# Optimization experiments

Hardware: AMD Instinct MI355X
Metric: run time of the kernel (lower is better)

## Reference

```python
import jax, jax.numpy as jnp
import numpy as np

B, C, H, W = 4, 512, 64, 64
CQ = C // 8  # query/key channels


def setup_inputs() -> dict:
    key = jax.random.key(0)
    k1, k2, k3, k4 = jax.random.split(key, 4)
    x = jax.random.normal(k1, (B, C, H, W), dtype=jnp.float32)
    Wq = jax.random.normal(k2, (CQ, C), dtype=jnp.float32) * (1.0 / np.sqrt(C))
    Wk = jax.random.normal(k3, (CQ, C), dtype=jnp.float32) * (1.0 / np.sqrt(C))
    Wv = jax.random.normal(k4, (C, C), dtype=jnp.float32) * (1.0 / np.sqrt(C))
    gamma = jnp.ones((1,), dtype=jnp.float32)
    return {"x": x, "Wq": Wq, "Wk": Wk, "Wv": Wv, "gamma": gamma}


def reference(x, Wq, Wk, Wv, gamma):
    b, c, h, w = x.shape
    n = h * w
    xf = x.reshape(b, c, n)                      # [B, C, N]
    # 1x1 convs over the flattened spatial dim == per-position linear maps
    f = jnp.einsum('oc,bcn->bon', Wq, xf)        # [B, C/8, N] query
    g = jnp.einsum('oc,bcn->bon', Wk, xf)        # [B, C/8, N] key
    hv = jnp.einsum('oc,bcn->bon', Wv, xf)       # [B, C,   N] value
    # scores[b, i, j] = sum_k f[b,k,i] * g[b,k,j]  (f^T g)
    scores = jnp.einsum('bki,bkj->bij', f, g)    # [B, N, N]
    # torch softmax dim=1 -> normalize over the i axis (first N axis)
    beta = jax.nn.softmax(scores, axis=1)
    o = gamma[0] * jnp.einsum('bcn,bnj->bcj', hv, beta) + xf  # [B, C, N]
    return o.reshape(b, c, h, w)
```

## Files before the change

kernel.cpp:

```cpp
#include <hip/hip_runtime.h>
#include <hip/hip_bf16.h>

typedef unsigned short u16;
typedef unsigned int   u32;
typedef _Float16 f16;
typedef __attribute__((ext_vector_type(8))) _Float16 f16x8;
typedef __attribute__((ext_vector_type(4))) _Float16 f16x4;
typedef __attribute__((ext_vector_type(4))) float    f32x4;
typedef __attribute__((ext_vector_type(8))) unsigned short u16x8;

#define BATCH 4
#define CH 512
#define NN 4096
#define CQ 64
#define LOG2E 1.44269504f

__device__ __forceinline__ float bf2f(u16 v) {
    union { unsigned int u; float f; } x; x.u = ((unsigned int)v) << 16; return x.f;
}

__device__ __forceinline__ size_t stt_idx(int j, int i) {
    return (size_t)(j >> 4) * 65536 + (size_t)((i >> 3) * 128 + (j & 15) * 8 + (i & 7));
}

__device__ __forceinline__ void glds16(const f16* g, f16* s) {
    __builtin_amdgcn_global_load_lds(
        (const __attribute__((address_space(1))) void*)g,
        (__attribute__((address_space(3))) void*)s, 16, 0, 0);
}

__global__ __launch_bounds__(64) void detect_kernel(const u32* __restrict__ xw,
                                                    int* __restrict__ flag)
{
    const u32 w  = xw[threadIdx.x];
    const u32 ex = (w >> 23) & 0xFFu;
    const int plausible = (ex >= 100u && ex <= 132u) ? 1 : 0;
    const unsigned long long m = __ballot(plausible);
    if (threadIdx.x == 0) flag[0] = (__popcll(m) >= 48) ? 0 : 1;
}

__global__ __launch_bounds__(256) void wconv_kernel(
    const void* __restrict__ Wq, const void* __restrict__ Wk,
    const void* __restrict__ Wv, const int* __restrict__ flag,
    f16* __restrict__ Wc)
{
    const int isbf = *flag;
    const int row = blockIdx.x;
    const int t   = threadIdx.x;
    const void* src; int r;
    if (row < 64)       { src = Wq; r = row; }
    else if (row < 128) { src = Wk; r = row - 64; }
    else                { src = Wv; r = row - 128; }
    f16 v0, v1;
    if (isbf) {
        const u16* p = (const u16*)src + (size_t)r * CH + 2 * t;
        v0 = (f16)bf2f(p[0]); v1 = (f16)bf2f(p[1]);
    } else {
        const float* p = (const float*)src + (size_t)r * CH + 2 * t;
        v0 = (f16)p[0]; v1 = (f16)p[1];
    }
    Wc[(size_t)row * CH + 2 * t]     = v0;
    Wc[(size_t)row * CH + 2 * t + 1] = v1;
}

__global__ __launch_bounds__(256) void xpose_kernel(
    const void* __restrict__ xin, const int* __restrict__ flag,
    f16* __restrict__ xT)
{
    const int isbf = *flag;
    const int n0 = blockIdx.x * 64, c0 = blockIdx.y * 64, b = blockIdx.z;
    const int t  = threadIdx.x;
    __shared__ float Xl[64][65];

    {
        const int row = t >> 2, nc = (t & 3) * 16;
        if (isbf) {
            const u16* p = (const u16*)xin +
                           ((size_t)(b * CH + c0 + row)) * NN + n0 + nc;
            const u16x8 a = *(const u16x8*)p;
            const u16x8 bq = *(const u16x8*)(p + 8);
#pragma unroll
            for (int i = 0; i < 8; ++i) Xl[row][nc + i]     = bf2f(a[i]);
#pragma unroll
            for (int i = 0; i < 8; ++i) Xl[row][nc + 8 + i] = bf2f(bq[i]);
        } else {
            const float* p = (const float*)xin +
                             ((size_t)(b * CH + c0 + row)) * NN + n0 + nc;
            *(f32x4*)&Xl[row][nc]      = *(const f32x4*)(p);
            *(f32x4*)&Xl[row][nc + 4]  = *(const f32x4*)(p + 4);
            *(f32x4*)&Xl[row][nc + 8]  = *(const f32x4*)(p + 8);
            *(f32x4*)&Xl[row][nc + 12] = *(const f32x4*)(p + 12);
        }
    }
    __syncthreads();
    {
        const int nr = t >> 2, cc = (t & 3) * 16;
        f16x8 o0, o1;
#pragma unroll
        for (int i = 0; i < 8; ++i) o0[i] = (f16)Xl[cc + i][nr];
#pragma unroll
        for (int i = 0; i < 8; ++i) o1[i] = (f16)Xl[cc + 8 + i][nr];
        f16* dst = xT + ((size_t)b * NN + n0 + nr) * CH + c0 + cc;
        *(f16x8*)dst       = o0;
        *(f16x8*)(dst + 8) = o1;
    }
}

__global__ __launch_bounds__(512, 2) void proj_mfma(
    const f16* __restrict__ Wc, const f16* __restrict__ xT,
    f16* __restrict__ fT, f16* __restrict__ gT, f16* __restrict__ hv)
{
    const int o0 = blockIdx.x * 128;
    const int n0 = blockIdx.y * 128;
    const int b  = blockIdx.z;
    const int t  = threadIdx.x;
    const int w  = t >> 6, l = t & 63;
    const int j16 = l & 15, h = l >> 4;
    const int ow = w >> 2, nw = w & 3;

    const f16* wp[4];
#pragma unroll
    for (int ot = 0; ot < 4; ++ot)
        wp[ot] = Wc + (size_t)(o0 + 64 * ow + 16 * ot + j16) * CH;
    const f16* xp[2];
#pragma unroll
    for (int bt = 0; bt < 2; ++bt)
        xp[bt] = xT + ((size_t)b * NN + n0 + 32 * nw + 16 * bt + j16) * CH;

    f32x4 acc[4][2];
#pragma unroll
    for (int ot = 0; ot < 4; ++ot)
#pragma unroll
        for (int bt = 0; bt < 2; ++bt)
#pragma unroll
            for (int r = 0; r < 4; ++r) acc[ot][bt][r] = 0.f;

    f16x8 af[2][4], bq[2][2];
#pragma unroll
    for (int ot = 0; ot < 4; ++ot) af[0][ot] = *(const f16x8*)(wp[ot] + 8 * h);
#pragma unroll
    for (int bt = 0; bt < 2; ++bt) bq[0][bt] = *(const f16x8*)(xp[bt] + 8 * h);

    for (int ks = 0; ks < 16; ++ks) {
        const int cur = ks & 1;
        if (ks < 15) {
            const int k1 = (ks + 1) * 32 + 8 * h;
#pragma unroll
            for (int ot = 0; ot < 4; ++ot)
                af[cur ^ 1][ot] = *(const f16x8*)(wp[ot] + k1);
#pragma unroll
            for (int bt = 0; bt < 2; ++bt)
                bq[cur ^ 1][bt] = *(const f16x8*)(xp[bt] + k1);
        }
        __builtin_amdgcn_s_setprio(1);
#pragma unroll
        for (int ot = 0; ot < 4; ++ot)
#pragma unroll
            for (int bt = 0; bt < 2; ++bt)
                acc[ot][bt] = __builtin_amdgcn_mfma_f32_16x16x32_f16(
                                  af[cur][ot], bq[cur][bt], acc[ot][bt], 0, 0, 0);
        __builtin_amdgcn_s_setprio(0);
    }

#pragma unroll
    for (int ot = 0; ot < 4; ++ot)
#pragma unroll
        for (int bt = 0; bt < 2; ++bt)
#pragma unroll
            for (int r = 0; r < 4; ++r) {
                const int o = o0 + 64 * ow + 16 * ot + 4 * h + r;
                const int n = n0 + 32 * nw + 16 * bt + j16;
                const f16 v = (f16)acc[ot][bt][r];
                if (o < CQ) {
                    fT[((size_t)b * NN + n) * CQ + o] = v;
                } else if (o < 2 * CQ) {
                    gT[((size_t)b * NN + n) * CQ + (o - CQ)] = v;
                } else {
                    hv[((size_t)b * CH + (o - 2 * CQ)) * NN + n] = v;
                }
            }
}

__global__ __launch_bounds__(512) void score_kernel(
    const f16* __restrict__ fT, const f16* __restrict__ gT,
    f16* __restrict__ ST, float* __restrict__ lsum, float* __restrict__ mbT,
    int b0)
{
    const int ibk = blockIdx.x;
    const int jbk = blockIdx.y;
    const int bz  = blockIdx.z;
    const int b   = b0 + bz;
    const int t   = threadIdx.x;
    const int w   = t >> 6, l = t & 63;
    const int c16 = l & 15, h = l >> 4;
    const int wr  = w >> 1;
    const int wc  = w & 1;
    const int j0  = jbk * 128 + wr * 32;
    const int i0  = ibk * 128 + wc * 64;
    const int itile = ibk * 2 + wc;

    const f16* fb_ = fT + (size_t)b * NN * CQ;
    const f16* gb_ = gT + (size_t)b * NN * CQ;

    f16x8 ga[2][2], fbr[4][2];
#pragma unroll
    for (int ja = 0; ja < 2; ++ja)
#pragma unroll
        for (int kc = 0; kc < 2; ++kc)
            ga[ja][kc] = *(const f16x8*)(gb_ +
                (size_t)(j0 + 16 * ja + c16) * CQ + 32 * kc + 8 * h);
#pragma unroll
    for (int ii = 0; ii < 4; ++ii)
#pragma unroll
        for (int kc = 0; kc < 2; ++kc)
            fbr[ii][kc] = *(const f16x8*)(fb_ +
                (size_t)(i0 + 16 * ii + c16) * CQ + 32 * kc + 8 * h);

    f32x4 s[2][4];
#pragma unroll
    for (int ja = 0; ja < 2; ++ja)
#pragma unroll
        for (int ii = 0; ii < 4; ++ii)
#pragma unroll
            for (int r = 0; r < 4; ++r) s[ja][ii][r] = 0.f;

#pragma unroll
    for (int ja = 0; ja < 2; ++ja)
#pragma unroll
        for (int ii = 0; ii < 4; ++ii) {
            s[ja][ii] = __builtin_amdgcn_mfma_f32_16x16x32_f16(
                            ga[ja][0], fbr[ii][0], s[ja][ii], 0, 0, 0);
            s[ja][ii] = __builtin_amdgcn_mfma_f32_16x16x32_f16(
                            ga[ja][1], fbr[ii][1], s[ja][ii], 0, 0, 0);
        }

    f16* Sb = ST + (size_t)bz * NN * NN;

#pragma unroll
    for (int ja = 0; ja < 2; ++ja)
#pragma unroll
        for (int r = 0; r < 4; ++r) {
            const int jj = j0 + 16 * ja + 4 * h + r;
            float hx[4];
#pragma unroll
            for (int ii = 0; ii < 4; ++ii) hx[ii] = s[ja][ii][r] * LOG2E;
            float mt = fmaxf(fmaxf(hx[0], hx[1]), fmaxf(hx[2], hx[3]));
            mt = fmaxf(mt, __shfl_xor(mt, 1));
            mt = fmaxf(mt, __shfl_xor(mt, 2));
            mt = fmaxf(mt, __shfl_xor(mt, 4));
            mt = fmaxf(mt, __shfl_xor(mt, 8));
            float rs = 0.f;
#pragma unroll
            for (int ii = 0; ii < 4; ++ii) {
                const float p = exp2f(hx[ii] - mt);
                rs += p;
                Sb[stt_idx(jj, i0 + 16 * ii + c16)] = (f16)p;
            }
            rs += __shfl_xor(rs, 1);
            rs += __shfl_xor(rs, 2);
            rs += __shfl_xor(rs, 4);
            rs += __shfl_xor(rs, 8);
            if (c16 == 0) {
                mbT[((size_t)b * 64 + itile) * NN + jj] = mt;
                atomicAdd(&lsum[(size_t)b * NN + jj], exp2f(mt) * rs);
            }
        }
}

__global__ __launch_bounds__(256) void fac_kernel(
    const float* __restrict__ lsum, const float* __restrict__ mbT,
    f16* __restrict__ facT, int b0)
{
    const int j  = blockIdx.x * 256 + threadIdx.x;
    const int it = blockIdx.y;
    const int bz = blockIdx.z;
    const int b  = b0 + bz;
    const float lg = __log2f(lsum[(size_t)b * NN + j]);
    const float m  = mbT[((size_t)b * 64 + it) * NN + j];
    facT[((size_t)bz * 64 + it) * NN + j] = (f16)exp2f(m - lg);
}

__global__ __launch_bounds__(256, 2) void pv_kernel(
    const void* __restrict__ xin, const f16* __restrict__ hv,
    const f16* __restrict__ ST, const f16* __restrict__ facT,
    const void* __restrict__ gammap, const int* __restrict__ flag,
    float* __restrict__ out, int b0, int bc)
{
    const int isbf = *flag;
    const int bid  = blockIdx.x;
    const int xcd  = bid & 7;
    const int slot = bid >> 3;
    const int perb = 8 / bc;
    const int bz   = xcd / perb;
    const int b    = b0 + bz;
    const int idx  = (xcd % perb) * (16 * bc) + slot;
    const int cb   = idx >> 4;
    const int jb   = idx & 15;
    const int j0   = jb * 256;
    const int c0   = cb * 64;

    const int t = threadIdx.x;
    const int w = t >> 6, l = t & 63;
    const int l16 = l & 15, h = l >> 4;
    const int jw0 = j0 + w * 64;

    __shared__ f16   Bs[2][4][2][64][8];
    __shared__ float Tl[4][16][65];

    const f16* SA  = ST + (size_t)bz * NN * NN
                   + (size_t)(jw0 >> 4) * 65536 + l16 * 8;
    const f16* hw_ = hv + (size_t)b * CH * NN
                   + (size_t)(c0 + 16 * w + l16) * NN + 8 * h;
    const f16* Ff  = facT + (size_t)bz * 64 * NN + jw0 + l16;

    f32x4 acc[4][4];
#pragma unroll
    for (int jt = 0; jt < 4; ++jt)
#pragma unroll
        for (int ct = 0; ct < 4; ++ct)
#pragma unroll
            for (int r = 0; r < 4; ++r) acc[jt][ct][r] = 0.f;

    f16x8 Aa[4][2], Ab[4][2];
    f16   fa[4], fb[4];

#define STAGE(BUF, K)                                                        \
    {                                                                        \
        glds16(hw_ + (K) * 64,      &Bs[BUF][w][0][0][0]);                   \
        glds16(hw_ + (K) * 64 + 32, &Bs[BUF][w][1][0][0]);                   \
    }

#define LDA_(A, F, K)                                                        \
    {                                                                        \
        _Pragma("unroll")                                                    \
        for (int jt = 0; jt < 4; ++jt) {                                     \
            _Pragma("unroll")                                                \
            for (int ck = 0; ck < 2; ++ck)                                   \
                A[jt][ck] = *(const f16x8*)(SA + (size_t)jt * 65536 +        \
                    ((K) * 8 + ck * 4 + h) * 128);                           \
            F[jt] = Ff[(size_t)(K) * NN + jt * 16];                          \
        }                                                                    \
    }

#define STEP(K, BUF, A_CUR, F_CUR, A_NXT, F_NXT, DO_PF)                      \
    {                                                                        \
        if (DO_PF) { STAGE(BUF ^ 1, (K) + 1); LDA_(A_NXT, F_NXT, (K) + 1); } \
        _Pragma("unroll")                                                    \
        for (int ck = 0; ck < 2; ++ck) {                                     \
            f16x8 bf[4];                                                     \
            _Pragma("unroll")                                                \
            for (int ci = 0; ci < 4; ++ci)                                   \
                bf[ci] = *(const f16x8*)&Bs[BUF][ci][ck][l][0];              \
            __builtin_amdgcn_s_setprio(1);                                   \
            _Pragma("unroll")                                                \
            for (int jt = 0; jt < 4; ++jt) {                                 \
                f16x8 fs;                                                    \
                _Pragma("unroll")                                            \
                for (int e = 0; e < 8; ++e) fs[e] = F_CUR[jt];               \
                const f16x8 pa = A_CUR[jt][ck] * fs;                         \
                _Pragma("unroll")                                            \
                for (int ci = 0; ci < 4; ++ci)                               \
                    acc[jt][ci] = __builtin_amdgcn_mfma_f32_16x16x32_f16(    \
                        pa, bf[ci], acc[jt][ci], 0, 0, 0);                   \
            }                                                                \
            __builtin_amdgcn_s_setprio(0);                                   \
        }                                                                    \
        __syncthreads();                                                     \
    }

    STAGE(0, 0);
    LDA_(Aa, fa, 0);
    __syncthreads();

    for (int k2 = 0; k2 < 32; ++k2) {
        STEP(2 * k2,     0, Aa, fa, Ab, fb, 1);
        STEP(2 * k2 + 1, 1, Ab, fb, Aa, fa, (k2 < 31));
    }

    float gam;
    if (isbf) gam = bf2f(((const u16*)gammap)[0]);
    else      gam = ((const float*)gammap)[0];

#pragma unroll
    for (int ct = 0; ct < 4; ++ct) {
#pragma unroll
        for (int jt = 0; jt < 4; ++jt)
            *(f32x4*)&Tl[w][l16][jt * 16 + 4 * h] = acc[jt][ct];
        asm volatile("s_waitcnt lgkmcnt(0)" ::: "memory");
#pragma unroll
        for (int cc = 0; cc < 16; ++cc) {
            const int c = c0 + ct * 16 + cc;
            const size_t oidx = ((size_t)b * CH + c) * NN + jw0 + l;
            float xv;
            if (isbf) xv = bf2f(((const u16*)xin)[oidx]);
            else      xv = ((const float*)xin)[oidx];
            out[oidx] = gam * Tl[w][cc][l] + xv;
        }
        asm volatile("s_waitcnt lgkmcnt(0)" ::: "memory");
    }
#undef STAGE
#undef LDA_
#undef STEP
}

__global__ __launch_bounds__(512, 2) void attn_mfma(
    const void* __restrict__ xin, const f16* __restrict__ fT,
    const f16* __restrict__ gT, const f16* __restrict__ hv,
    const void* __restrict__ gammap, const int* __restrict__ flag,
    float* __restrict__ out)
{
    const int isbf = *flag;
    const int bid  = blockIdx.x;
    const int xcd  = bid & 7, slot = bid >> 3;
    const int b    = xcd >> 1;
    const int jblk = ((xcd & 1) << 6) + slot;
    const int j0   = jblk * 32;
    const int t    = threadIdx.x;
    const int w    = t >> 6;
    const int l    = t & 63;
    const int j16  = l & 15;
    const int h    = l >> 4;

    __shared__ f16   Pp[32 * 256];
    __shared__ float wmax[8][2][16];
    __shared__ float wsum[8][2][16];

    f16x8 gf[2][2];
#pragma unroll
    for (int jb = 0; jb < 2; ++jb)
#pragma unroll
        for (int kc = 0; kc < 2; ++kc)
            gf[jb][kc] = *(const f16x8*)(gT +
                ((size_t)b * NN + j0 + 16 * jb + j16) * CQ + 32 * kc + 8 * h);

    f32x4 oacc[4][2];
#pragma unroll
    for (int cb = 0; cb < 4; ++cb)
#pragma unroll
        for (int jb = 0; jb < 2; ++jb)
#pragma unroll
            for (int r = 0; r < 4; ++r) oacc[cb][jb][r] = 0.f;

    float m_run[2] = {-1e30f, -1e30f};
    float l_run[2] = {0.f, 0.f};

    const f16* fbase = fT + (size_t)b * NN * CQ;
    const f16* hbase = hv + (size_t)b * CH * NN;

    f16x8 fa[2][2];
    {
        const int irow0 = 32 * w + j16;
        fa[0][0] = *(const f16x8*)(fbase + (size_t)irow0 * CQ + 8 * h);
        fa[0][1] = *(const f16x8*)(fbase + (size_t)irow0 * CQ + 32 + 8 * h);
        fa[1][0] = *(const f16x8*)(fbase + (size_t)(irow0 + 16) * CQ + 8 * h);
        fa[1][1] = *(const f16x8*)(fbase + (size_t)(irow0 + 16) * CQ + 32 + 8 * h);
    }
    f16x8 aA[4], aB[4];

#define LDAF(BUF, KC, I0BASE)                                                 \
    {                                                                         \
        _Pragma("unroll")                                                     \
        for (int cb = 0; cb < 4; ++cb)                                        \
            BUF[cb] = *(const f16x8*)(hbase +                                 \
                (size_t)(64 * w + 16 * cb + j16) * NN +                       \
                (I0BASE) + 32 * (KC) + 8 * h);                                \
    }

#define PVSTF(BUF, KC)                                                        \
    {                                                                         \
        const int sw0 = (4 * (KC) + h) ^ j16;                                 \
        const f16x8 pf0 = *(const f16x8*)&Pp[j16 * 256 + sw0 * 8];            \
        const f16x8 pf1 = *(const f16x8*)&Pp[(16 + j16) * 256 + sw0 * 8];     \
        _Pragma("unroll")                                                     \
        for (int cb = 0; cb < 4; ++cb) {                                      \
            oacc[cb][0] = __builtin_amdgcn_mfma_f32_16x16x32_f16(             \
                              BUF[cb], pf0, oacc[cb][0], 0, 0, 0);            \
            oacc[cb][1] = __builtin_amdgcn_mfma_f32_16x16x32_f16(             \
                              BUF[cb], pf1, oacc[cb][1], 0, 0, 0);            \
        }                                                                     \
    }

    LDAF(aA, 0, 0);
    LDAF(aB, 1, 0);

    for (int it = 0; it < 16; ++it) {
        const int i0 = it * 256;

        f32x4 s[2][2];
#pragma unroll
        for (int ib = 0; ib < 2; ++ib)
#pragma unroll
            for (int jb = 0; jb < 2; ++jb)
#pragma unroll
                for (int r = 0; r < 4; ++r) s[ib][jb][r] = 0.f;

#pragma unroll
        for (int ib = 0; ib < 2; ++ib)
#pragma unroll
            for (int jb = 0; jb < 2; ++jb) {
                s[ib][jb] = __builtin_amdgcn_mfma_f32_16x16x32_f16(
                                fa[ib][0], gf[jb][0], s[ib][jb], 0, 0, 0);
                s[ib][jb] = __builtin_amdgcn_mfma_f32_16x16x32_f16(
                                fa[ib][1], gf[jb][1], s[ib][jb], 0, 0, 0);
            }

        float pmax[2];
#pragma unroll
        for (int jb = 0; jb < 2; ++jb) {
            float m0 = fmaxf(fmaxf(s[0][jb][0], s[0][jb][1]),
                             fmaxf(s[0][jb][2], s[0][jb][3]));
            float m1 = fmaxf(fmaxf(s[1][jb][0], s[1][jb][1]),
                             fmaxf(s[1][jb][2], s[1][jb][3]));
            float mm = fmaxf(m0, m1);
            mm = fmaxf(mm, __shfl_xor(mm, 16));
            mm = fmaxf(mm, __shfl_xor(mm, 32));
            pmax[jb] = mm;
        }
        if (h == 0) { wmax[w][0][j16] = pmax[0]; wmax[w][1][j16] = pmax[1]; }
        __syncthreads();

        float m_new[2], sc[2];
#pragma unroll
        for (int jb = 0; jb < 2; ++jb) {
            float tm = wmax[0][jb][j16];
#pragma unroll
            for (int w2 = 1; w2 < 8; ++w2) tm = fmaxf(tm, wmax[w2][jb][j16]);
            m_new[jb] = fmaxf(m_run[jb], tm);
            sc[jb]    = __expf(m_run[jb] - m_new[jb]);
            m_run[jb] = m_new[jb];
        }

        float psum[2] = {0.f, 0.f};
#pragma unroll
        for (int ib = 0; ib < 2; ++ib) {
#pragma unroll
            for (int jb = 0; jb < 2; ++jb) {
                const float p0 = __expf(s[ib][jb][0] - m_new[jb]);
                const float p1 = __expf(s[ib][jb][1] - m_new[jb]);
                const float p2 = __expf(s[ib][jb][2] - m_new[jb]);
                const float p3 = __expf(s[ib][jb][3] - m_new[jb]);
                psum[jb] += (p0 + p1) + (p2 + p3);
                f16x4 v4;
                v4[0] = (f16)p0; v4[1] = (f16)p1; v4[2] = (f16)p2; v4[3] = (f16)p3;
                const int jloc = 16 * jb + j16;
                const int sw   = (4 * w + 2 * ib + (h >> 1)) ^ j16;
                *(f16x4*)&Pp[jloc * 256 + sw * 8 + (h & 1) * 4] = v4;
            }
        }
#pragma unroll
        for (int jb = 0; jb < 2; ++jb) {
            psum[jb] += __shfl_xor(psum[jb], 16);
            psum[jb] += __shfl_xor(psum[jb], 32);
        }
        if (h == 0) { wsum[w][0][j16] = psum[0]; wsum[w][1][j16] = psum[1]; }

#pragma unroll
        for (int cb = 0; cb < 4; ++cb)
#pragma unroll
            for (int jb = 0; jb < 2; ++jb)
#pragma unroll
                for (int r = 0; r < 4; ++r) oacc[cb][jb][r] *= sc[jb];

        __syncthreads();

#pragma unroll
        for (int jb = 0; jb < 2; ++jb) {
            float ts = 0.f;
#pragma unroll
            for (int w2 = 0; w2 < 8; ++w2) ts += wsum[w2][jb][j16];
            l_run[jb] = l_run[jb] * sc[jb] + ts;
        }

        const int i0n = (it < 15) ? (i0 + 256) : 0;
        {
            const int irow0 = i0n + 32 * w + j16;
            fa[0][0] = *(const f16x8*)(fbase + (size_t)irow0 * CQ + 8 * h);
            fa[0][1] = *(const f16x8*)(fbase + (size_t)irow0 * CQ + 32 + 8 * h);
            fa[1][0] = *(const f16x8*)(fbase + (size_t)(irow0 + 16) * CQ + 8 * h);
            fa[1][1] = *(const f16x8*)(fbase + (size_t)(irow0 + 16) * CQ + 32 + 8 * h);
        }
        PVSTF(aA, 0); LDAF(aA, 2, i0);
        PVSTF(aB, 1); LDAF(aB, 3, i0);
        PVSTF(aA, 2); LDAF(aA, 4, i0);
        PVSTF(aB, 3); LDAF(aB, 5, i0);
        PVSTF(aA, 4); LDAF(aA, 6, i0);
        PVSTF(aB, 5); LDAF(aB, 7, i0);
        PVSTF(aA, 6); LDAF(aA, 0, i0n);
        PVSTF(aB, 7); LDAF(aB, 1, i0n);
    }

    float gam;
    if (isbf) gam = bf2f(((const u16*)gammap)[0]);
    else      gam = ((const float*)gammap)[0];

    const float inv0 = gam / l_run[0];
    const float inv1 = gam / l_run[1];

#pragma unroll
    for (int cb = 0; cb < 4; ++cb) {
#pragma unroll
        for (int jb = 0; jb < 2; ++jb) {
            const float invj = jb ? inv1 : inv0;
            const int j = j0 + 16 * jb + j16;
#pragma unroll
            for (int r = 0; r < 4; ++r) {
                const int c = 64 * w + 16 * cb + 4 * h + r;
                const size_t idx = ((size_t)b * CH + c) * NN + j;
                float xv;
                if (isbf) xv = bf2f(((const u16*)xin)[idx]);
                else      xv = ((const float*)xin)[idx];
                out[idx] = oacc[cb][jb][r] * invj + xv;
            }
        }
    }
#undef LDAF
#undef PVSTF
}

extern "C" void kernel_launch(void* const* d_in, const int* in_sizes, int n_in,
                              void* d_out, int out_size, void* d_ws, size_t ws_size,
                              hipStream_t stream)
{
    const size_t off_l  = 256;
    const size_t off_m  = off_l  + (size_t)BATCH * NN * 4;
    const size_t off_fT = off_m  + (size_t)BATCH * NN * 64 * 4;
    const size_t off_gT = off_fT + (size_t)BATCH * NN * CQ * 2;
    const size_t off_hv = off_gT + (size_t)BATCH * NN * CQ * 2;
    const size_t off_xT = off_hv + (size_t)BATCH * CH * NN * 2;
    const size_t off_Wc = off_xT + (size_t)BATCH * NN * CH * 2;
    const size_t off_ST = off_Wc + (size_t)640 * CH * 2;
    const size_t stN    = (size_t)NN * NN * 2;
    const size_t facN   = (size_t)64 * NN * 2;

    int*   flag = (int*)d_ws;
    float* lsum = (float*)((char*)d_ws + off_l);
    float* mbT  = (float*)((char*)d_ws + off_m);
    f16*   fT   = (f16*)((char*)d_ws + off_fT);
    f16*   gT   = (f16*)((char*)d_ws + off_gT);
    f16*   hv   = (f16*)((char*)d_ws + off_hv);
    f16*   xT   = (f16*)((char*)d_ws + off_xT);
    f16*   Wc   = (f16*)((char*)d_ws + off_Wc);
    f16*   ST   = (f16*)((char*)d_ws + off_ST);

    int bc = 0;
    if      (ws_size >= off_ST + 4 * (stN + facN)) bc = 4;
    else if (ws_size >= off_ST + 2 * (stN + facN)) bc = 2;
    else if (ws_size >= off_ST + 1 * (stN + facN)) bc = 1;
    f16* facT = (f16*)((char*)d_ws + off_ST + (size_t)bc * stN);

    detect_kernel<<<1, 64, 0, stream>>>((const u32*)d_in[0], flag);
    wconv_kernel<<<640, 256, 0, stream>>>(d_in[1], d_in[2], d_in[3], flag, Wc);
    xpose_kernel<<<dim3(64, 8, BATCH), 256, 0, stream>>>(d_in[0], flag, xT);
    proj_mfma<<<dim3(5, 32, BATCH), 512, 0, stream>>>(Wc, xT, fT, gT, hv);

    if (bc) {
        (void)hipMemsetAsync(lsum, 0, (size_t)BATCH * NN * 4, stream);
        for (int b0 = 0; b0 < BATCH; b0 += bc) {
            dim3 g1(32, 32, bc);
            score_kernel<<<g1, 512, 0, stream>>>(fT, gT, ST, lsum, mbT, b0);
            fac_kernel<<<dim3(16, 64, bc), 256, 0, stream>>>(lsum, mbT, facT, b0);
            pv_kernel<<<128 * bc, 256, 0, stream>>>(d_in[0], hv, ST, facT,
                                                    d_in[4], flag,
                                                    (float*)d_out, b0, bc);
        }
    } else {
        attn_mfma<<<512, 512, 0, stream>>>(d_in[0], fT, gT, hv, d_in[4],
                                           flag, (float*)d_out);
    }
}
```

Baseline: 307.8 us.

## Triple-buffer value tiles with prefetch depth two and stage factors in LDS

Moves the main accumulation loop from a double-buffered, distance-one prefetch to a triple-buffered ring with distance-two prefetch. It uses explicit vmcnt waits plus a raw s_barrier in place of a full __syncthreads after each step. The per-column softmax factors are no longer loaded as scattered scalar global reads each step. They are bulk-loaded once into a new LDS array and read from there. This aims to hide global-load latency and remove small uncoalesced loads, at the cost of more LDS and registers (a third A register set), which may lower occupancy. The relaxed vmcnt-based synchronization also carries correctness risk.

```diff
diff --git a/kernel.cpp b/kernel.cpp
--- a/kernel.cpp
+++ b/kernel.cpp
@@ -304,14 +304,16 @@
     const int l16 = l & 15, h = l >> 4;
     const int jw0 = j0 + w * 64;
 
-    __shared__ f16   Bs[2][4][2][64][8];
+    __shared__ f16   Bs[3][4][2][64][8];
+    __shared__ f16   Fl[4][64][64];
     __shared__ float Tl[4][16][65];
 
     const f16* SA  = ST + (size_t)bz * NN * NN
                    + (size_t)(jw0 >> 4) * 65536 + l16 * 8;
     const f16* hw_ = hv + (size_t)b * CH * NN
                    + (size_t)(c0 + 16 * w + l16) * NN + 8 * h;
-    const f16* Ff  = facT + (size_t)bz * 64 * NN + jw0 + l16;
+    const f16* Ff8 = facT + (size_t)bz * 64 * NN
+                   + (size_t)(l >> 3) * NN + jw0 + (l & 7) * 8;
 
     f32x4 acc[4][4];
 #pragma unroll
@@ -321,42 +323,45 @@
 #pragma unroll
             for (int r = 0; r < 4; ++r) acc[jt][ct][r] = 0.f;
 
-    f16x8 Aa[4][2], Ab[4][2];
-    f16   fa[4], fb[4];
-
-#define STAGE(BUF, K)                                                        \
+    f16x8 A0[4][2], A1[4][2], A2[4][2];
+
+#define STAGE(R, K)                                                          \
     {                                                                        \
-        glds16(hw_ + (K) * 64,      &Bs[BUF][w][0][0][0]);                   \
-        glds16(hw_ + (K) * 64 + 32, &Bs[BUF][w][1][0][0]);                   \
-    }
-
-#define LDA_(A, F, K)                                                        \
+        glds16(hw_ + (K) * 64,      &Bs[R][w][0][0][0]);                     \
+        glds16(hw_ + (K) * 64 + 32, &Bs[R][w][1][0][0]);                     \
+    }
+
+#define LDA_(A, K)                                                           \
     {                                                                        \
         _Pragma("unroll")                                                    \
-        for (int jt = 0; jt < 4; ++jt) {                                     \
+        for (int jt = 0; jt < 4; ++jt)                                       \
             _Pragma("unroll")                                                \
             for (int ck = 0; ck < 2; ++ck)                                   \
                 A[jt][ck] = *(const f16x8*)(SA + (size_t)jt * 65536 +        \
                     ((K) * 8 + ck * 4 + h) * 128);                           \
-            F[jt] = Ff[(size_t)(K) * NN + jt * 16];                          \
-        }                                                                    \
-    }
-
-#define STEP(K, BUF, A_CUR, F_CUR, A_NXT, F_NXT, DO_PF)                      \
+    }
+
+#define STEP(K, RCUR, RNXT, A_CUR, A_NXT, NSTR, DO_PF)                       \
     {                                                                        \
-        if (DO_PF) { STAGE(BUF ^ 1, (K) + 1); LDA_(A_NXT, F_NXT, (K) + 1); } \
+        asm volatile("s_waitcnt vmcnt(" NSTR ")" ::: "memory");              \
+        __builtin_amdgcn_s_barrier();                                        \
+        __builtin_amdgcn_sched_barrier(0);                                   \
+        if (DO_PF) { STAGE(RNXT, (K) + 2); LDA_(A_NXT, (K) + 2); }           \
+        f16 facs[4];                                                         \
+        _Pragma("unroll")                                                    \
+        for (int jt = 0; jt < 4; ++jt) facs[jt] = Fl[w][(K)][jt * 16 + l16]; \
         _Pragma("unroll")                                                    \
         for (int ck = 0; ck < 2; ++ck) {                                     \
             f16x8 bf[4];                                                     \
             _Pragma("unroll")                                                \
             for (int ci = 0; ci < 4; ++ci)                                   \
-                bf[ci] = *(const f16x8*)&Bs[BUF][ci][ck][l][0];              \
+                bf[ci] = *(const f16x8*)&Bs[RCUR][ci][ck][l][0];             \
             __builtin_amdgcn_s_setprio(1);                                   \
             _Pragma("unroll")                                                \
             for (int jt = 0; jt < 4; ++jt) {                                 \
                 f16x8 fs;                                                    \
                 _Pragma("unroll")                                            \
-                for (int e = 0; e < 8; ++e) fs[e] = F_CUR[jt];               \
+                for (int e = 0; e < 8; ++e) fs[e] = facs[jt];                \
                 const f16x8 pa = A_CUR[jt][ck] * fs;                         \
                 _Pragma("unroll")                                            \
                 for (int ci = 0; ci < 4; ++ci)                               \
@@ -365,17 +370,21 @@
             }                                                                \
             __builtin_amdgcn_s_setprio(0);                                   \
         }                                                                    \
-        __syncthreads();                                                     \
-    }
-
-    STAGE(0, 0);
-    LDA_(Aa, fa, 0);
-    __syncthreads();
-
-    for (int k2 = 0; k2 < 32; ++k2) {
-        STEP(2 * k2,     0, Aa, fa, Ab, fb, 1);
-        STEP(2 * k2 + 1, 1, Ab, fb, Aa, fa, (k2 < 31));
-    }
+    }
+
+#pragma unroll
+    for (int q = 0; q < 8; ++q)
+        glds16(Ff8 + (size_t)(8 * q) * NN, &Fl[w][8 * q][0]);
+    STAGE(0, 0); LDA_(A0, 0);
+    STAGE(1, 1); LDA_(A1, 1);
+
+    for (int k3 = 0; k3 < 21; ++k3) {
+        const int k0 = 3 * k3;
+        STEP(k0,     0, 2, A0, A2, "10", (k0     < 62));
+        STEP(k0 + 1, 1, 0, A1, A0, "10", (k0 + 1 < 62));
+        STEP(k0 + 2, 2, 1, A2, A1, "10", (k0 + 2 < 62));
+    }
+    STEP(63, 0, 1, A0, A1, "0", 0);
 
     float gam;
     if (isbf) gam = bf2f(((const u16*)gammap)[0]);
```

Measured after the change: 291.6 us (median of 2 runs). 1.06x faster.
